# Kernel optimization log

Hardware: AMD Instinct MI355X
Metric: run time of the kernel (lower is better)

Reference implementation:

```python
import jax, jax.numpy as jnp
import numpy as np

N_EMBD = 64
HEAD_SIZE = 64
BLOCK_SIZE = 256

def setup_inputs() -> dict:
    key = jax.random.key(0)
    ks = jax.random.split(key, 7)
    B, T, C = 2048, 256, N_EMBD
    scale = 1.0 / np.sqrt(C)
    inputs = jax.random.normal(ks[0], (B, T, C), dtype=jnp.float32)
    Wk = jax.random.uniform(ks[1], (C, HEAD_SIZE), jnp.float32, -scale, scale)
    bk = jax.random.uniform(ks[2], (HEAD_SIZE,), jnp.float32, -scale, scale)
    Wq = jax.random.uniform(ks[3], (C, HEAD_SIZE), jnp.float32, -scale, scale)
    bq = jax.random.uniform(ks[4], (HEAD_SIZE,), jnp.float32, -scale, scale)
    Wv = jax.random.uniform(ks[5], (C, HEAD_SIZE), jnp.float32, -scale, scale)
    bv = jax.random.uniform(ks[6], (HEAD_SIZE,), jnp.float32, -scale, scale)
    return {"inputs": inputs, "Wk": Wk, "bk": bk, "Wq": Wq, "bq": bq, "Wv": Wv, "bv": bv}

def reference(inputs, Wk, bk, Wq, bq, Wv, bv):
    T = inputs.shape[1]
    k = inputs @ Wk + bk          # [B,T,H]
    q = inputs @ Wq + bq          # [B,T,H]
    v = inputs @ Wv + bv          # [B,T,H]
    scores = jnp.einsum('bqh,bkh->bqk', q, k) / jnp.sqrt(jnp.asarray(k.shape[-1], k.dtype))
    causal = jnp.tril(jnp.ones((T, T), dtype=bool))
    scores = jnp.where(causal, scores, -jnp.inf)
    attn = jax.nn.softmax(scores, axis=-1)
    return jnp.einsum('bqk,bkh->bqh', attn, v)
```

## Files before the change

kernel.cpp:

```cpp
#include <hip/hip_runtime.h>

typedef short s8v __attribute__((ext_vector_type(8)));
typedef short s4v __attribute__((ext_vector_type(4)));
typedef float f4v __attribute__((ext_vector_type(4)));
typedef unsigned int u32;

#define MFMA16(a,b,c) __builtin_amdgcn_mfma_f32_16x16x32_bf16((a),(b),(c),0,0,0)

__device__ __forceinline__ unsigned short f2bf(float x) {
  union { float f; unsigned u; } v; v.f = x;
  unsigned r = v.u + 0x7FFFu + ((v.u >> 16) & 1u);
  return (unsigned short)(r >> 16);
}

__device__ __forceinline__ u32 cvtpk(float lo, float hi) {
  u32 r;
  asm("v_cvt_pk_bf16_f32 %0, %1, %2" : "=v"(r) : "v"(lo), "v"(hi));
  return r;
}

__global__ void prep_wt(const float* __restrict__ Wk, const float* __restrict__ Wq,
                        const float* __restrict__ Wv, unsigned short* __restrict__ WT) {
  int i = blockIdx.x * 256 + threadIdx.x;
  if (i >= 64 * 64) return;
  int n = i >> 6, k = i & 63;
  WT[i]            = f2bf(Wk[k * 64 + n]);
  WT[4096 + i]     = f2bf(Wq[k * 64 + n] * (0.125f * 1.44269504f));
  WT[2 * 4096 + i] = f2bf(Wv[k * 64 + n]);
}

__global__ __launch_bounds__(512, 4) void head_fused(
    const float* __restrict__ X, const unsigned short* __restrict__ WT,
    const float* __restrict__ bk, const float* __restrict__ bq,
    const float* __restrict__ bv, float* __restrict__ Out)
{
  __shared__ char lds[65536];
  char* Kl = lds;
  char* Vt = lds + 32768;
  const int tid  = threadIdx.x;
  const int wave = tid >> 6;
  const int lane = tid & 63;
  const int lrow = lane & 15;
  const int lgrp = lane >> 4;
  char* scw = Kl + wave * 4096;

  const float* Xb = X + (size_t)blockIdx.x * (256 * 64);
  float* Ob = Out + (size_t)blockIdx.x * (256 * 64);

  auto xfrag = [&](int tt, int kk) -> s8v {
    const float* p = Xb + (tt * 16 + lrow) * 64 + kk * 32 + lgrp * 8;
    f4v a = *(const f4v*)p;
    f4v b = *(const f4v*)(p + 4);
    s8v f;
    f[0] = (short)f2bf(a[0]); f[1] = (short)f2bf(a[1]);
    f[2] = (short)f2bf(a[2]); f[3] = (short)f2bf(a[3]);
    f[4] = (short)f2bf(b[0]); f[5] = (short)f2bf(b[1]);
    f[6] = (short)f2bf(b[2]); f[7] = (short)f2bf(b[3]);
    return f;
  };

  s8v qf[2][2];
  {
    float biasq[4];
#pragma unroll
    for (int nt = 0; nt < 4; ++nt) biasq[nt] = bq[nt * 16 + lrow] * (0.125f * 1.44269504f);
    s8v wfQ[4][2];
#pragma unroll
    for (int nt = 0; nt < 4; ++nt)
#pragma unroll
      for (int kk = 0; kk < 2; ++kk)
        wfQ[nt][kk] = *(const s8v*)(WT + 4096 + (nt * 16 + lrow) * 64 + kk * 32 + lgrp * 8);
#pragma unroll
    for (int i = 0; i < 2; ++i) {
      const int t = i ? (15 - wave) : wave;
      const s8v x0 = xfrag(t, 0);
      const s8v x1 = xfrag(t, 1);
#pragma unroll
      for (int nt = 0; nt < 4; ++nt) {
        f4v a = {0.f, 0.f, 0.f, 0.f};
        a = MFMA16(x0, wfQ[nt][0], a);
        a = MFMA16(x1, wfQ[nt][1], a);
#pragma unroll
        for (int r = 0; r < 4; ++r) {
          const int row = lgrp * 4 + r;
          const int off = (row * 128 + (nt * 16 + lrow) * 2) ^ ((row & 7) << 4);
          *(unsigned short*)(scw + off) = f2bf(a[r] + biasq[nt]);
        }
      }
      asm volatile("s_waitcnt lgkmcnt(0)" ::: "memory");
      qf[i][0] = *(const s8v*)(scw + ((lrow * 128 + lgrp * 16) ^ ((lrow & 7) << 4)));
      qf[i][1] = *(const s8v*)(scw + ((lrow * 128 + 64 + lgrp * 16) ^ ((lrow & 7) << 4)));
    }
  }

  {
    float biask[4], biasv[4];
#pragma unroll
    for (int nt = 0; nt < 4; ++nt) {
      biask[nt] = bk[nt * 16 + lrow];
      biasv[nt] = bv[nt * 16 + lrow];
    }
#pragma unroll
    for (int it = 0; it < 2; ++it) {
      const int tt = wave * 2 + it;
      const s8v x0 = xfrag(tt, 0);
      const s8v x1 = xfrag(tt, 1);
#pragma unroll
      for (int nt = 0; nt < 4; ++nt) {
        const s8v wk0 = *(const s8v*)(WT + (nt * 16 + lrow) * 64 + lgrp * 8);
        const s8v wk1 = *(const s8v*)(WT + (nt * 16 + lrow) * 64 + 32 + lgrp * 8);
        const s8v wv0 = *(const s8v*)(WT + 2 * 4096 + (nt * 16 + lrow) * 64 + lgrp * 8);
        const s8v wv1 = *(const s8v*)(WT + 2 * 4096 + (nt * 16 + lrow) * 64 + 32 + lgrp * 8);
        f4v aK = {0.f, 0.f, 0.f, 0.f};
        aK = MFMA16(x0, wk0, aK);
        aK = MFMA16(x1, wk1, aK);
#pragma unroll
        for (int r = 0; r < 4; ++r) {
          const int row = tt * 16 + lgrp * 4 + r;
          const int off = (row * 128 + (nt * 16 + lrow) * 2) ^ ((row & 7) << 4);
          *(unsigned short*)(Kl + off) = f2bf(aK[r] + biask[nt]);
        }
        f4v aV = {0.f, 0.f, 0.f, 0.f};
        aV = MFMA16(x0, wv0, aV);
        aV = MFMA16(x1, wv1, aV);
        const int h = nt * 16 + lrow;
        s4v pk;
#pragma unroll
        for (int r = 0; r < 4; ++r) pk[r] = (short)f2bf(aV[r] + biasv[nt]);
        const int tp = (tt >> 1) * 32 + 8 * lgrp + 4 * (tt & 1);
        const int offv = (h * 512 + tp * 2) ^ ((h & 7) << 4);
        *(s4v*)(Vt + offv) = pk;
      }
    }
  }

  __syncthreads();

#pragma unroll
  for (int i = 0; i < 2; ++i) {
    const int t = i ? (15 - wave) : wave;
    const int nblk = (t >> 1) + 1;
    const int qrow = t * 16 + lrow;
    f4v Oa[4];
#pragma unroll
    for (int nt = 0; nt < 4; ++nt) Oa[nt] = (f4v){0.f, 0.f, 0.f, 0.f};
    float mm = -1e30f, ll = 0.f;

    for (int b2 = 0; b2 < nblk; ++b2) {
      f4v S0 = {0.f, 0.f, 0.f, 0.f}, S1 = {0.f, 0.f, 0.f, 0.f};
      __builtin_amdgcn_s_setprio(1);
#pragma unroll
      for (int kk = 0; kk < 2; ++kk) {
        const s8v kf0 = *(const s8v*)(Kl + (((b2 * 32 + lrow) * 128 + kk * 64 + lgrp * 16) ^ ((lrow & 7) << 4)));
        const s8v kf1 = *(const s8v*)(Kl + (((b2 * 32 + 16 + lrow) * 128 + kk * 64 + lgrp * 16) ^ ((lrow & 7) << 4)));
        S0 = MFMA16(kf0, qf[i][kk], S0);
        S1 = MFMA16(kf1, qf[i][kk], S1);
      }
      __builtin_amdgcn_s_setprio(0);
      if (b2 == nblk - 1) {
#pragma unroll
        for (int r = 0; r < 4; ++r) {
          const int k0 = b2 * 32 + lgrp * 4 + r;
          if (k0 > qrow)      S0[r] = -1e30f;
          if (k0 + 16 > qrow) S1[r] = -1e30f;
        }
      }
      float pm = fmaxf(fmaxf(fmaxf(S0[0], S0[1]), fmaxf(S0[2], S0[3])),
                       fmaxf(fmaxf(S1[0], S1[1]), fmaxf(S1[2], S1[3])));
      pm = fmaxf(pm, __shfl_xor(pm, 16));
      pm = fmaxf(pm, __shfl_xor(pm, 32));
      const float mn = fmaxf(mm, pm);
      const float sc = __builtin_amdgcn_exp2f(mm - mn);
      mm = mn;
#pragma unroll
      for (int r = 0; r < 4; ++r) {
        S0[r] = __builtin_amdgcn_exp2f(S0[r] - mn);
        S1[r] = __builtin_amdgcn_exp2f(S1[r] - mn);
      }
      float rs = ((S0[0] + S0[1]) + (S0[2] + S0[3])) + ((S1[0] + S1[1]) + (S1[2] + S1[3]));
      rs += __shfl_xor(rs, 16);
      rs += __shfl_xor(rs, 32);
      ll = ll * sc + rs;
      union { u32 u[4]; s8v v; } pu;
      pu.u[0] = cvtpk(S0[0], S0[1]);
      pu.u[1] = cvtpk(S0[2], S0[3]);
      pu.u[2] = cvtpk(S1[0], S1[1]);
      pu.u[3] = cvtpk(S1[2], S1[3]);
#pragma unroll
      for (int nt = 0; nt < 4; ++nt)
#pragma unroll
        for (int r = 0; r < 4; ++r) Oa[nt][r] *= sc;
      __builtin_amdgcn_s_setprio(1);
#pragma unroll
      for (int nt = 0; nt < 4; ++nt) {
        const s8v vf = *(const s8v*)(Vt + (((nt * 16 + lrow) * 512 + b2 * 64 + lgrp * 16) ^ ((lrow & 7) << 4)));
        Oa[nt] = MFMA16(vf, pu.v, Oa[nt]);
      }
      __builtin_amdgcn_s_setprio(0);
    }
    const float inv = 1.0f / ll;
#pragma unroll
    for (int nt = 0; nt < 4; ++nt) {
      f4v o;
#pragma unroll
      for (int r = 0; r < 4; ++r) o[r] = Oa[nt][r] * inv;
      *(f4v*)(Ob + (size_t)qrow * 64 + nt * 16 + lgrp * 4) = o;
    }
  }
}

extern "C" void kernel_launch(void* const* d_in, const int* in_sizes, int n_in,
                              void* d_out, int out_size, void* d_ws, size_t ws_size,
                              hipStream_t stream) {
  const float* X  = (const float*)d_in[0];
  const float* Wk = (const float*)d_in[1];
  const float* bk = (const float*)d_in[2];
  const float* Wq = (const float*)d_in[3];
  const float* bq = (const float*)d_in[4];
  const float* Wv = (const float*)d_in[5];
  const float* bv = (const float*)d_in[6];
  float* Out = (float*)d_out;
  unsigned short* WT = (unsigned short*)d_ws;

  const int B = in_sizes[0] / (256 * 64);
  prep_wt<<<dim3(16), dim3(256), 0, stream>>>(Wk, Wq, Wv, WT);
  head_fused<<<dim3(B), dim3(512), 0, stream>>>(X, WT, bk, bq, bv, Out);
}
```

Before: 123.1 us.

## Fuse both query tiles into one KV loop with lazy rescaling and packed bf16 converts

Merges the two per-wave query tiles (t and 15-t) into a single loop over key blocks. Each K and V fragment loaded from LDS now feeds both tiles' MFMAs, which halves LDS reads and gives the scheduler two independent chains to interleave. Softmax rescaling is skipped unless the running max grows by more than 8 (in log2 units), and the scalar bf16 rounding is replaced with packed v_cvt_pk_bf16_f32 conversions in the projections. The Q scratch writes are double-buffered so only one wait is needed. The cost is higher register pressure from two sets of accumulators, and the lazy rescale leaves exp values up to 2^8 before conversion to bf16.

```diff
diff --git a/kernel.cpp b/kernel.cpp
--- a/kernel.cpp
+++ b/kernel.cpp
@@ -42,7 +42,6 @@
   const int lane = tid & 63;
   const int lrow = lane & 15;
   const int lgrp = lane >> 4;
-  char* scw = Kl + wave * 4096;
 
   const float* Xb = X + (size_t)blockIdx.x * (256 * 64);
   float* Ob = Out + (size_t)blockIdx.x * (256 * 64);
@@ -51,12 +50,10 @@
     const float* p = Xb + (tt * 16 + lrow) * 64 + kk * 32 + lgrp * 8;
     f4v a = *(const f4v*)p;
     f4v b = *(const f4v*)(p + 4);
-    s8v f;
-    f[0] = (short)f2bf(a[0]); f[1] = (short)f2bf(a[1]);
-    f[2] = (short)f2bf(a[2]); f[3] = (short)f2bf(a[3]);
-    f[4] = (short)f2bf(b[0]); f[5] = (short)f2bf(b[1]);
-    f[6] = (short)f2bf(b[2]); f[7] = (short)f2bf(b[3]);
-    return f;
+    union { u32 u[4]; s8v v; } r;
+    r.u[0] = cvtpk(a[0], a[1]); r.u[1] = cvtpk(a[2], a[3]);
+    r.u[2] = cvtpk(b[0], b[1]); r.u[3] = cvtpk(b[2], b[3]);
+    return r.v;
   };
 
   s8v qf[2][2];
@@ -73,6 +70,7 @@
 #pragma unroll
     for (int i = 0; i < 2; ++i) {
       const int t = i ? (15 - wave) : wave;
+      char* scw = Kl + wave * 4096 + i * 2048;
       const s8v x0 = xfrag(t, 0);
       const s8v x1 = xfrag(t, 1);
 #pragma unroll
@@ -80,14 +78,22 @@
         f4v a = {0.f, 0.f, 0.f, 0.f};
         a = MFMA16(x0, wfQ[nt][0], a);
         a = MFMA16(x1, wfQ[nt][1], a);
+        const u32 c01 = cvtpk(a[0] + biasq[nt], a[1] + biasq[nt]);
+        const u32 c23 = cvtpk(a[2] + biasq[nt], a[3] + biasq[nt]);
+        const int col2 = (nt * 16 + lrow) * 2;
 #pragma unroll
         for (int r = 0; r < 4; ++r) {
           const int row = lgrp * 4 + r;
-          const int off = (row * 128 + (nt * 16 + lrow) * 2) ^ ((row & 7) << 4);
-          *(unsigned short*)(scw + off) = f2bf(a[r] + biasq[nt]);
+          const int off = (row * 128 + col2) ^ ((row & 7) << 4);
+          const u32 w = (r < 2) ? c01 : c23;
+          *(unsigned short*)(scw + off) = (unsigned short)((r & 1) ? (w >> 16) : (w & 0xffff));
         }
       }
-      asm volatile("s_waitcnt lgkmcnt(0)" ::: "memory");
+    }
+    asm volatile("s_waitcnt lgkmcnt(0)" ::: "memory");
+#pragma unroll
+    for (int i = 0; i < 2; ++i) {
+      char* scw = Kl + wave * 4096 + i * 2048;
       qf[i][0] = *(const s8v*)(scw + ((lrow * 128 + lgrp * 16) ^ ((lrow & 7) << 4)));
       qf[i][1] = *(const s8v*)(scw + ((lrow * 128 + 64 + lgrp * 16) ^ ((lrow & 7) << 4)));
     }
@@ -114,98 +120,134 @@
         f4v aK = {0.f, 0.f, 0.f, 0.f};
         aK = MFMA16(x0, wk0, aK);
         aK = MFMA16(x1, wk1, aK);
+        const u32 k01 = cvtpk(aK[0] + biask[nt], aK[1] + biask[nt]);
+        const u32 k23 = cvtpk(aK[2] + biask[nt], aK[3] + biask[nt]);
+        const int col2 = (nt * 16 + lrow) * 2;
 #pragma unroll
         for (int r = 0; r < 4; ++r) {
           const int row = tt * 16 + lgrp * 4 + r;
-          const int off = (row * 128 + (nt * 16 + lrow) * 2) ^ ((row & 7) << 4);
-          *(unsigned short*)(Kl + off) = f2bf(aK[r] + biask[nt]);
+          const int off = (row * 128 + col2) ^ ((row & 7) << 4);
+          const u32 w = (r < 2) ? k01 : k23;
+          *(unsigned short*)(Kl + off) = (unsigned short)((r & 1) ? (w >> 16) : (w & 0xffff));
         }
         f4v aV = {0.f, 0.f, 0.f, 0.f};
         aV = MFMA16(x0, wv0, aV);
         aV = MFMA16(x1, wv1, aV);
         const int h = nt * 16 + lrow;
-        s4v pk;
-#pragma unroll
-        for (int r = 0; r < 4; ++r) pk[r] = (short)f2bf(aV[r] + biasv[nt]);
+        union { u32 u[2]; s4v v; } pk;
+        pk.u[0] = cvtpk(aV[0] + biasv[nt], aV[1] + biasv[nt]);
+        pk.u[1] = cvtpk(aV[2] + biasv[nt], aV[3] + biasv[nt]);
         const int tp = (tt >> 1) * 32 + 8 * lgrp + 4 * (tt & 1);
         const int offv = (h * 512 + tp * 2) ^ ((h & 7) << 4);
-        *(s4v*)(Vt + offv) = pk;
+        *(s4v*)(Vt + offv) = pk.v;
       }
     }
   }
 
   __syncthreads();
 
-#pragma unroll
-  for (int i = 0; i < 2; ++i) {
-    const int t = i ? (15 - wave) : wave;
-    const int nblk = (t >> 1) + 1;
-    const int qrow = t * 16 + lrow;
-    f4v Oa[4];
-#pragma unroll
-    for (int nt = 0; nt < 4; ++nt) Oa[nt] = (f4v){0.f, 0.f, 0.f, 0.f};
-    float mm = -1e30f, ll = 0.f;
-
-    for (int b2 = 0; b2 < nblk; ++b2) {
-      f4v S0 = {0.f, 0.f, 0.f, 0.f}, S1 = {0.f, 0.f, 0.f, 0.f};
-      __builtin_amdgcn_s_setprio(1);
-#pragma unroll
-      for (int kk = 0; kk < 2; ++kk) {
-        const s8v kf0 = *(const s8v*)(Kl + (((b2 * 32 + lrow) * 128 + kk * 64 + lgrp * 16) ^ ((lrow & 7) << 4)));
-        const s8v kf1 = *(const s8v*)(Kl + (((b2 * 32 + 16 + lrow) * 128 + kk * 64 + lgrp * 16) ^ ((lrow & 7) << 4)));
-        S0 = MFMA16(kf0, qf[i][kk], S0);
-        S1 = MFMA16(kf1, qf[i][kk], S1);
-      }
-      __builtin_amdgcn_s_setprio(0);
-      if (b2 == nblk - 1) {
-#pragma unroll
-        for (int r = 0; r < 4; ++r) {
-          const int k0 = b2 * 32 + lgrp * 4 + r;
-          if (k0 > qrow)      S0[r] = -1e30f;
-          if (k0 + 16 > qrow) S1[r] = -1e30f;
-        }
-      }
-      float pm = fmaxf(fmaxf(fmaxf(S0[0], S0[1]), fmaxf(S0[2], S0[3])),
-                       fmaxf(fmaxf(S1[0], S1[1]), fmaxf(S1[2], S1[3])));
-      pm = fmaxf(pm, __shfl_xor(pm, 16));
-      pm = fmaxf(pm, __shfl_xor(pm, 32));
+  const int t0 = wave, t1 = 15 - wave;
+  const int nb0 = (t0 >> 1) + 1, nb1 = (t1 >> 1) + 1;
+  const int q0r = t0 * 16 + lrow, q1r = t1 * 16 + lrow;
+
+  auto maskdiag = [&](f4v& S0, f4v& S1, int qrow, int rb) {
+#pragma unroll
+    for (int r = 0; r < 4; ++r) {
+      const int k0 = rb + lgrp * 4 + r;
+      if (k0 > qrow)      S0[r] = -1e30f;
+      if (k0 + 16 > qrow) S1[r] = -1e30f;
+    }
+  };
+  auto softmax_pack = [&](f4v& S0, f4v& S1, float& mm, float& ll, f4v* Oa) -> s8v {
+    float pm = fmaxf(fmaxf(fmaxf(S0[0], S0[1]), fmaxf(S0[2], S0[3])),
+                     fmaxf(fmaxf(S1[0], S1[1]), fmaxf(S1[2], S1[3])));
+    pm = fmaxf(pm, __shfl_xor(pm, 16));
+    pm = fmaxf(pm, __shfl_xor(pm, 32));
+    if (!__all(pm <= mm + 8.f)) {
       const float mn = fmaxf(mm, pm);
       const float sc = __builtin_amdgcn_exp2f(mm - mn);
       mm = mn;
-#pragma unroll
-      for (int r = 0; r < 4; ++r) {
-        S0[r] = __builtin_amdgcn_exp2f(S0[r] - mn);
-        S1[r] = __builtin_amdgcn_exp2f(S1[r] - mn);
-      }
-      float rs = ((S0[0] + S0[1]) + (S0[2] + S0[3])) + ((S1[0] + S1[1]) + (S1[2] + S1[3]));
-      rs += __shfl_xor(rs, 16);
-      rs += __shfl_xor(rs, 32);
-      ll = ll * sc + rs;
-      union { u32 u[4]; s8v v; } pu;
-      pu.u[0] = cvtpk(S0[0], S0[1]);
-      pu.u[1] = cvtpk(S0[2], S0[3]);
-      pu.u[2] = cvtpk(S1[0], S1[1]);
-      pu.u[3] = cvtpk(S1[2], S1[3]);
+      ll *= sc;
 #pragma unroll
       for (int nt = 0; nt < 4; ++nt)
 #pragma unroll
         for (int r = 0; r < 4; ++r) Oa[nt][r] *= sc;
-      __builtin_amdgcn_s_setprio(1);
-#pragma unroll
-      for (int nt = 0; nt < 4; ++nt) {
-        const s8v vf = *(const s8v*)(Vt + (((nt * 16 + lrow) * 512 + b2 * 64 + lgrp * 16) ^ ((lrow & 7) << 4)));
-        Oa[nt] = MFMA16(vf, pu.v, Oa[nt]);
-      }
-      __builtin_amdgcn_s_setprio(0);
-    }
-    const float inv = 1.0f / ll;
-#pragma unroll
-    for (int nt = 0; nt < 4; ++nt) {
-      f4v o;
-#pragma unroll
-      for (int r = 0; r < 4; ++r) o[r] = Oa[nt][r] * inv;
-      *(f4v*)(Ob + (size_t)qrow * 64 + nt * 16 + lgrp * 4) = o;
-    }
+    }
+#pragma unroll
+    for (int r = 0; r < 4; ++r) {
+      S0[r] = __builtin_amdgcn_exp2f(S0[r] - mm);
+      S1[r] = __builtin_amdgcn_exp2f(S1[r] - mm);
+    }
+    float rs = ((S0[0] + S0[1]) + (S0[2] + S0[3])) + ((S1[0] + S1[1]) + (S1[2] + S1[3]));
+    rs += __shfl_xor(rs, 16);
+    rs += __shfl_xor(rs, 32);
+    ll += rs;
+    union { u32 u[4]; s8v v; } pu;
+    pu.u[0] = cvtpk(S0[0], S0[1]);
+    pu.u[1] = cvtpk(S0[2], S0[3]);
+    pu.u[2] = cvtpk(S1[0], S1[1]);
+    pu.u[3] = cvtpk(S1[2], S1[3]);
+    return pu.v;
+  };
+
+  f4v Oa0[4], Oa1[4];
+  float mm0 = -1e30f, ll0 = 0.f, mm1 = -1e30f, ll1 = 0.f;
+#pragma unroll
+  for (int nt = 0; nt < 4; ++nt) {
+    Oa0[nt] = (f4v){0.f, 0.f, 0.f, 0.f};
+    Oa1[nt] = (f4v){0.f, 0.f, 0.f, 0.f};
+  }
+
+  for (int b2 = 0; b2 < nb1; ++b2) {
+    const bool d0 = (b2 < nb0);
+    const int rb = b2 * 32;
+    const s8v kf0a = *(const s8v*)(Kl + (((rb + lrow) * 128 + lgrp * 16) ^ ((lrow & 7) << 4)));
+    const s8v kf0b = *(const s8v*)(Kl + (((rb + lrow) * 128 + 64 + lgrp * 16) ^ ((lrow & 7) << 4)));
+    const s8v kf1a = *(const s8v*)(Kl + (((rb + 16 + lrow) * 128 + lgrp * 16) ^ ((lrow & 7) << 4)));
+    const s8v kf1b = *(const s8v*)(Kl + (((rb + 16 + lrow) * 128 + 64 + lgrp * 16) ^ ((lrow & 7) << 4)));
+    f4v S10 = {0.f,0.f,0.f,0.f}, S11 = {0.f,0.f,0.f,0.f};
+    f4v S00 = {0.f,0.f,0.f,0.f}, S01 = {0.f,0.f,0.f,0.f};
+    __builtin_amdgcn_s_setprio(1);
+    S10 = MFMA16(kf0a, qf[1][0], S10); S10 = MFMA16(kf0b, qf[1][1], S10);
+    S11 = MFMA16(kf1a, qf[1][0], S11); S11 = MFMA16(kf1b, qf[1][1], S11);
+    if (d0) {
+      S00 = MFMA16(kf0a, qf[0][0], S00); S00 = MFMA16(kf0b, qf[0][1], S00);
+      S01 = MFMA16(kf1a, qf[0][0], S01); S01 = MFMA16(kf1b, qf[0][1], S01);
+    }
+    __builtin_amdgcn_s_setprio(0);
+    if (b2 == nb1 - 1) maskdiag(S10, S11, q1r, rb);
+    s8v p1 = softmax_pack(S10, S11, mm1, ll1, Oa1);
+    s8v p0;
+    if (d0) {
+      if (b2 == nb0 - 1) maskdiag(S00, S01, q0r, rb);
+      p0 = softmax_pack(S00, S01, mm0, ll0, Oa0);
+    }
+    const s8v vf0 = *(const s8v*)(Vt + (((0 * 16 + lrow) * 512 + b2 * 64 + lgrp * 16) ^ ((lrow & 7) << 4)));
+    const s8v vf1 = *(const s8v*)(Vt + (((1 * 16 + lrow) * 512 + b2 * 64 + lgrp * 16) ^ ((lrow & 7) << 4)));
+    const s8v vf2 = *(const s8v*)(Vt + (((2 * 16 + lrow) * 512 + b2 * 64 + lgrp * 16) ^ ((lrow & 7) << 4)));
+    const s8v vf3 = *(const s8v*)(Vt + (((3 * 16 + lrow) * 512 + b2 * 64 + lgrp * 16) ^ ((lrow & 7) << 4)));
+    __builtin_amdgcn_s_setprio(1);
+    Oa1[0] = MFMA16(vf0, p1, Oa1[0]);
+    Oa1[1] = MFMA16(vf1, p1, Oa1[1]);
+    Oa1[2] = MFMA16(vf2, p1, Oa1[2]);
+    Oa1[3] = MFMA16(vf3, p1, Oa1[3]);
+    if (d0) {
+      Oa0[0] = MFMA16(vf0, p0, Oa0[0]);
+      Oa0[1] = MFMA16(vf1, p0, Oa0[1]);
+      Oa0[2] = MFMA16(vf2, p0, Oa0[2]);
+      Oa0[3] = MFMA16(vf3, p0, Oa0[3]);
+    }
+    __builtin_amdgcn_s_setprio(0);
+  }
+
+  const float inv0 = 1.0f / ll0, inv1 = 1.0f / ll1;
+#pragma unroll
+  for (int nt = 0; nt < 4; ++nt) {
+    f4v o0, o1;
+#pragma unroll
+    for (int r = 0; r < 4; ++r) { o0[r] = Oa0[nt][r] * inv0; o1[r] = Oa1[nt][r] * inv1; }
+    *(f4v*)(Ob + (size_t)q0r * 64 + nt * 16 + lgrp * 4) = o0;
+    *(f4v*)(Ob + (size_t)q1r * 64 + nt * 16 + lgrp * 4) = o1;
   }
 }
 
```

Measured after the change: 143.5 us. 16.5% more time.

## Use packed bf16 conversions, lazy softmax rescale, and hoisted K/V fragment loads

Applied to the files above, without the earlier changes.

Replaces the scalar software f32-to-bf16 rounding with the hardware v_cvt_pk_bf16_f32 instruction when building the X, Q, K and V fragments. The online softmax now rescales O and l only when some row's running max would grow by more than 8 (log2 units), skipping the per-block multiply of the accumulators. The K and V LDS fragment loads are issued ahead of the MFMAs, and the Q scratch uses separate slots per tile so one wait covers both. The lazy rescale lets unnormalised exponentials reach up to 2^8, which stays within the range bf16 and f32 can hold but adds a wave-wide vote and a branch in the inner loop.

```diff
diff --git a/kernel.cpp b/kernel.cpp
--- a/kernel.cpp
+++ b/kernel.cpp
@@ -42,7 +42,6 @@
   const int lane = tid & 63;
   const int lrow = lane & 15;
   const int lgrp = lane >> 4;
-  char* scw = Kl + wave * 4096;
 
   const float* Xb = X + (size_t)blockIdx.x * (256 * 64);
   float* Ob = Out + (size_t)blockIdx.x * (256 * 64);
@@ -51,12 +50,10 @@
     const float* p = Xb + (tt * 16 + lrow) * 64 + kk * 32 + lgrp * 8;
     f4v a = *(const f4v*)p;
     f4v b = *(const f4v*)(p + 4);
-    s8v f;
-    f[0] = (short)f2bf(a[0]); f[1] = (short)f2bf(a[1]);
-    f[2] = (short)f2bf(a[2]); f[3] = (short)f2bf(a[3]);
-    f[4] = (short)f2bf(b[0]); f[5] = (short)f2bf(b[1]);
-    f[6] = (short)f2bf(b[2]); f[7] = (short)f2bf(b[3]);
-    return f;
+    union { u32 u[4]; s8v v; } r;
+    r.u[0] = cvtpk(a[0], a[1]); r.u[1] = cvtpk(a[2], a[3]);
+    r.u[2] = cvtpk(b[0], b[1]); r.u[3] = cvtpk(b[2], b[3]);
+    return r.v;
   };
 
   s8v qf[2][2];
@@ -73,6 +70,7 @@
 #pragma unroll
     for (int i = 0; i < 2; ++i) {
       const int t = i ? (15 - wave) : wave;
+      char* scw = Kl + wave * 4096 + i * 2048;
       const s8v x0 = xfrag(t, 0);
       const s8v x1 = xfrag(t, 1);
 #pragma unroll
@@ -80,17 +78,28 @@
         f4v a = {0.f, 0.f, 0.f, 0.f};
         a = MFMA16(x0, wfQ[nt][0], a);
         a = MFMA16(x1, wfQ[nt][1], a);
+        const u32 c01 = cvtpk(a[0] + biasq[nt], a[1] + biasq[nt]);
+        const u32 c23 = cvtpk(a[2] + biasq[nt], a[3] + biasq[nt]);
+        const int col2 = (nt * 16 + lrow) * 2;
 #pragma unroll
         for (int r = 0; r < 4; ++r) {
           const int row = lgrp * 4 + r;
-          const int off = (row * 128 + (nt * 16 + lrow) * 2) ^ ((row & 7) << 4);
-          *(unsigned short*)(scw + off) = f2bf(a[r] + biasq[nt]);
+          const int off = (row * 128 + col2) ^ ((row & 7) << 4);
+          const u32 w = (r < 2) ? c01 : c23;
+          *(unsigned short*)(scw + off) = (unsigned short)((r & 1) ? (w >> 16) : (w & 0xffff));
         }
       }
-      asm volatile("s_waitcnt lgkmcnt(0)" ::: "memory");
+    }
+    asm volatile("s_waitcnt lgkmcnt(0)" ::: "memory");
+    __builtin_amdgcn_sched_barrier(0);
+#pragma unroll
+    for (int i = 0; i < 2; ++i) {
+      char* scw = Kl + wave * 4096 + i * 2048;
       qf[i][0] = *(const s8v*)(scw + ((lrow * 128 + lgrp * 16) ^ ((lrow & 7) << 4)));
       qf[i][1] = *(const s8v*)(scw + ((lrow * 128 + 64 + lgrp * 16) ^ ((lrow & 7) << 4)));
     }
+    asm volatile("s_waitcnt lgkmcnt(0)" ::: "memory");
+    __builtin_amdgcn_sched_barrier(0);
   }
 
   {
@@ -114,22 +123,26 @@
         f4v aK = {0.f, 0.f, 0.f, 0.f};
         aK = MFMA16(x0, wk0, aK);
         aK = MFMA16(x1, wk1, aK);
+        const u32 k01 = cvtpk(aK[0] + biask[nt], aK[1] + biask[nt]);
+        const u32 k23 = cvtpk(aK[2] + biask[nt], aK[3] + biask[nt]);
+        const int col2 = (nt * 16 + lrow) * 2;
 #pragma unroll
         for (int r = 0; r < 4; ++r) {
           const int row = tt * 16 + lgrp * 4 + r;
-          const int off = (row * 128 + (nt * 16 + lrow) * 2) ^ ((row & 7) << 4);
-          *(unsigned short*)(Kl + off) = f2bf(aK[r] + biask[nt]);
+          const int off = (row * 128 + col2) ^ ((row & 7) << 4);
+          const u32 w = (r < 2) ? k01 : k23;
+          *(unsigned short*)(Kl + off) = (unsigned short)((r & 1) ? (w >> 16) : (w & 0xffff));
         }
         f4v aV = {0.f, 0.f, 0.f, 0.f};
         aV = MFMA16(x0, wv0, aV);
         aV = MFMA16(x1, wv1, aV);
         const int h = nt * 16 + lrow;
-        s4v pk;
-#pragma unroll
-        for (int r = 0; r < 4; ++r) pk[r] = (short)f2bf(aV[r] + biasv[nt]);
+        union { u32 u[2]; s4v v; } pk;
+        pk.u[0] = cvtpk(aV[0] + biasv[nt], aV[1] + biasv[nt]);
+        pk.u[1] = cvtpk(aV[2] + biasv[nt], aV[3] + biasv[nt]);
         const int tp = (tt >> 1) * 32 + 8 * lgrp + 4 * (tt & 1);
         const int offv = (h * 512 + tp * 2) ^ ((h & 7) << 4);
-        *(s4v*)(Vt + offv) = pk;
+        *(s4v*)(Vt + offv) = pk.v;
       }
     }
   }
@@ -147,57 +160,70 @@
     float mm = -1e30f, ll = 0.f;
 
     for (int b2 = 0; b2 < nblk; ++b2) {
-      f4v S0 = {0.f, 0.f, 0.f, 0.f}, S1 = {0.f, 0.f, 0.f, 0.f};
+      const int rb = b2 * 32;
+      const s8v kf0a = *(const s8v*)(Kl + (((rb + lrow) * 128 + lgrp * 16) ^ ((lrow & 7) << 4)));
+      const s8v kf0b = *(const s8v*)(Kl + (((rb + lrow) * 128 + 64 + lgrp * 16) ^ ((lrow & 7) << 4)));
+      const s8v kf1a = *(const s8v*)(Kl + (((rb + 16 + lrow) * 128 + lgrp * 16) ^ ((lrow & 7) << 4)));
+      const s8v kf1b = *(const s8v*)(Kl + (((rb + 16 + lrow) * 128 + 64 + lgrp * 16) ^ ((lrow & 7) << 4)));
+
+      f4v S0 = {0.f,0.f,0.f,0.f}, S1 = {0.f,0.f,0.f,0.f};
       __builtin_amdgcn_s_setprio(1);
-#pragma unroll
-      for (int kk = 0; kk < 2; ++kk) {
-        const s8v kf0 = *(const s8v*)(Kl + (((b2 * 32 + lrow) * 128 + kk * 64 + lgrp * 16) ^ ((lrow & 7) << 4)));
-        const s8v kf1 = *(const s8v*)(Kl + (((b2 * 32 + 16 + lrow) * 128 + kk * 64 + lgrp * 16) ^ ((lrow & 7) << 4)));
-        S0 = MFMA16(kf0, qf[i][kk], S0);
-        S1 = MFMA16(kf1, qf[i][kk], S1);
-      }
+      S0 = MFMA16(kf0a, qf[i][0], S0);
+      S0 = MFMA16(kf0b, qf[i][1], S0);
+      S1 = MFMA16(kf1a, qf[i][0], S1);
+      S1 = MFMA16(kf1b, qf[i][1], S1);
       __builtin_amdgcn_s_setprio(0);
+
       if (b2 == nblk - 1) {
 #pragma unroll
         for (int r = 0; r < 4; ++r) {
-          const int k0 = b2 * 32 + lgrp * 4 + r;
+          const int k0 = rb + lgrp * 4 + r;
           if (k0 > qrow)      S0[r] = -1e30f;
           if (k0 + 16 > qrow) S1[r] = -1e30f;
         }
       }
+
       float pm = fmaxf(fmaxf(fmaxf(S0[0], S0[1]), fmaxf(S0[2], S0[3])),
                        fmaxf(fmaxf(S1[0], S1[1]), fmaxf(S1[2], S1[3])));
       pm = fmaxf(pm, __shfl_xor(pm, 16));
       pm = fmaxf(pm, __shfl_xor(pm, 32));
-      const float mn = fmaxf(mm, pm);
-      const float sc = __builtin_amdgcn_exp2f(mm - mn);
-      mm = mn;
+      if (!__all(pm <= mm + 8.f)) {
+        const float mn = fmaxf(mm, pm);
+        const float sc = __builtin_amdgcn_exp2f(mm - mn);
+        mm = mn;
+        ll *= sc;
+#pragma unroll
+        for (int nt = 0; nt < 4; ++nt)
+#pragma unroll
+          for (int r = 0; r < 4; ++r) Oa[nt][r] *= sc;
+      }
 #pragma unroll
       for (int r = 0; r < 4; ++r) {
-        S0[r] = __builtin_amdgcn_exp2f(S0[r] - mn);
-        S1[r] = __builtin_amdgcn_exp2f(S1[r] - mn);
+        S0[r] = __builtin_amdgcn_exp2f(S0[r] - mm);
+        S1[r] = __builtin_amdgcn_exp2f(S1[r] - mm);
       }
       float rs = ((S0[0] + S0[1]) + (S0[2] + S0[3])) + ((S1[0] + S1[1]) + (S1[2] + S1[3]));
       rs += __shfl_xor(rs, 16);
       rs += __shfl_xor(rs, 32);
-      ll = ll * sc + rs;
+      ll += rs;
+
       union { u32 u[4]; s8v v; } pu;
       pu.u[0] = cvtpk(S0[0], S0[1]);
       pu.u[1] = cvtpk(S0[2], S0[3]);
       pu.u[2] = cvtpk(S1[0], S1[1]);
       pu.u[3] = cvtpk(S1[2], S1[3]);
+
+      s8v vf[4];
 #pragma unroll
       for (int nt = 0; nt < 4; ++nt)
-#pragma unroll
-        for (int r = 0; r < 4; ++r) Oa[nt][r] *= sc;
+        vf[nt] = *(const s8v*)(Vt + (((nt * 16 + lrow) * 512 + b2 * 64 + lgrp * 16) ^ ((lrow & 7) << 4)));
+
       __builtin_amdgcn_s_setprio(1);
 #pragma unroll
-      for (int nt = 0; nt < 4; ++nt) {
-        const s8v vf = *(const s8v*)(Vt + (((nt * 16 + lrow) * 512 + b2 * 64 + lgrp * 16) ^ ((lrow & 7) << 4)));
-        Oa[nt] = MFMA16(vf, pu.v, Oa[nt]);
-      }
+      for (int nt = 0; nt < 4; ++nt) Oa[nt] = MFMA16(vf[nt], pu.v, Oa[nt]);
       __builtin_amdgcn_s_setprio(0);
     }
+
     const float inv = 1.0f / ll;
 #pragma unroll
     for (int nt = 0; nt < 4; ++nt) {
```

Result: slower. 134.8 us (+9.5%).
